# Kernel optimization log

Measured on AMD Instinct MI355X. Metric: run time of the kernel, lower is better.

The kernel has to match this reference:

```python
import jax, jax.numpy as jnp
import numpy as np

HEADS = 16  # init kwarg 'heads'

def setup_inputs() -> dict:
    key = jax.random.key(0)
    k1, k2, k3 = jax.random.split(key, 3)
    B, S, D = 2, 2048, 1024
    x = jax.random.normal(k1, (B, S, D), dtype=jnp.float32)
    # nn.Linear(dim, 3*dim, bias=False): y = x @ W^T; store as [D, 3D] already transposed.
    w_qkv = jax.random.normal(k2, (D, 3 * D), dtype=jnp.float32) * 0.02
    w_out = jax.random.normal(k3, (D, D), dtype=jnp.float32) * 0.02
    return {"x": x, "w_qkv": w_qkv, "w_out": w_out}

def reference(x, w_qkv, w_out):
    B, S, D = x.shape
    H = HEADS
    hd = D // H
    scale = 1.0 / jnp.sqrt(jnp.asarray(hd, dtype=x.dtype))
    qkv = x @ w_qkv                      # [B, S, 3D]
    q, k, v = jnp.split(qkv, 3, axis=-1)
    def to_heads(t):
        return t.reshape(B, S, H, hd).transpose(0, 2, 1, 3)  # [B, H, S, hd]
    q, k, v = to_heads(q), to_heads(k), to_heads(v)
    scores = jnp.einsum('bhqd,bhkd->bhqk', q, k) * scale      # [B, H, S, S]
    # causal mask: query i attends to keys j <= i
    causal = jnp.tril(jnp.ones((S, S), dtype=bool))
    scores = jnp.where(causal, scores, -jnp.inf)
    p = jax.nn.softmax(scores, axis=-1)  # online-softmax in the original == exact softmax
    o = jnp.einsum('bhqk,bhkd->bhqd', p, v)                   # [B, H, S, hd]
    out = o.transpose(0, 2, 1, 3).reshape(B, S, D)
    return out @ w_out
```

## Files before the change

### kernel.cpp

```cpp
#include <hip/hip_runtime.h>


typedef unsigned short u16;
typedef unsigned int   u32;
typedef __attribute__((ext_vector_type(4))) u16    u16x4;
typedef __attribute__((ext_vector_type(8))) u16    u16x8;
typedef __attribute__((ext_vector_type(4))) short  s16x4;
typedef __attribute__((ext_vector_type(8))) __bf16 bf16x8;
typedef __attribute__((ext_vector_type(4))) float  f32x4;
typedef __attribute__((ext_vector_type(16))) float f32x16;

#define DEV static __device__ __forceinline__

DEV u16 f2b(float f) {
  unsigned u = __float_as_uint(f);
  u += 0x7fffu + ((u >> 16) & 1u);
  return (u16)(u >> 16);
}

DEV void gload_lds16(const void* g, void* l) {
  __builtin_amdgcn_global_load_lds((const __attribute__((address_space(1))) void*)g,
                                   (__attribute__((address_space(3))) void*)l, 16, 0, 0);
}

DEV unsigned lds_off(const void* p) {
  return (unsigned)(unsigned long long)(const __attribute__((address_space(3))) void*)p;
}

DEV s16x4 tr_read(unsigned off) {
  s16x4 d;
  asm volatile("ds_read_b64_tr_b16 %0, %1" : "=v"(d) : "v"(off));
  return d;
}

DEV u32 cvt_pk(float lo, float hi) {
  u32 r;
  asm("v_cvt_pk_bf16_f32 %0, %1, %2" : "=v"(r) : "v"(lo), "v"(hi));
  return r;
}

DEV void pswap(u32& x, u32& y) {
  asm volatile("v_permlane32_swap_b32 %0, %1" : "+v"(x), "+v"(y));
}

DEV f32x4 mfma32(bf16x8 a, bf16x8 b, f32x4 c) {
  return __builtin_amdgcn_mfma_f32_16x16x32_bf16(a, b, c, 0, 0, 0);
}
DEV f32x16 mfma3232(bf16x8 a, bf16x8 b, f32x16 c) {
  return __builtin_amdgcn_mfma_f32_32x32x16_bf16(a, b, c, 0, 0, 0);
}

__global__ __launch_bounds__(256) void cvt_kernel(const float* __restrict__ in,
                                                  u16* __restrict__ out, int n4) {
  int i = blockIdx.x * 256 + threadIdx.x;
  if (i >= n4) return;
  const float4 v = ((const float4*)in)[i];
  u16x4 o = { f2b(v.x), f2b(v.y), f2b(v.z), f2b(v.w) };
  ((u16x4*)out)[i] = o;
}

__global__ __launch_bounds__(256) void transpose_cvt(const float* __restrict__ w,
                                                     u16* __restrict__ wt,
                                                     const int Kdim, const int Ndim,
                                                     const int scaleN) {
  __shared__ u16 ls[32][33];
  const int tn = blockIdx.x * 32, tk = blockIdx.y * 32;
  const int t = threadIdx.x;
  const int r = t >> 3, c4 = (t & 7) * 4;
  const float s = (tn < scaleN) ? 0.18033688011112042f : 1.0f;
  float4 v = *(const float4*)(w + (size_t)(tk + r) * Ndim + tn + c4);
  ls[r][c4 + 0] = f2b(v.x * s); ls[r][c4 + 1] = f2b(v.y * s);
  ls[r][c4 + 2] = f2b(v.z * s); ls[r][c4 + 3] = f2b(v.w * s);
  __syncthreads();
  u16x4 ov = { ls[c4 + 0][r], ls[c4 + 1][r], ls[c4 + 2][r], ls[c4 + 3][r] };
  *(u16x4*)(wt + (size_t)(tn + r) * Kdim + tk + c4) = ov;
}

template<bool OUT_BF16>
__global__ __launch_bounds__(256) void gemm_bt(const u16* __restrict__ A,
                                               const u16* __restrict__ Bt,
                                               void* __restrict__ C, const int ldc) {
  const int gx = gridDim.x;
  const int id = (int)(blockIdx.y * gx + blockIdx.x);
  const int nxp = gx >> 3;
  const int xcd = id & 7, loc = id >> 3;
  const int tn = (xcd * nxp + loc % nxp) * 128;
  const int tm = (loc / nxp) * 128;
  const int tid = threadIdx.x;
  const int wave = tid >> 6, lane = tid & 63;
  const int wr = wave >> 1, wc = wave & 1;
  const int lg = lane >> 4, lc = lane & 15;
  __shared__ __align__(128) u16 lsA[128 * 32];
  __shared__ __align__(128) u16 lsB[128 * 32];

  f32x4 acc[4][4];
#pragma unroll
  for (int i = 0; i < 4; ++i)
#pragma unroll
    for (int j = 0; j < 4; ++j) acc[i][j] = (f32x4){0.f, 0.f, 0.f, 0.f};

  for (int kt = 0; kt < 32; ++kt) {
#pragma unroll
    for (int c = 0; c < 2; ++c) {
      const int p = tid + c * 256;
      const int row = p >> 2, ck = p & 3;
      const int cg = ck ^ ((row >> 1) & 3);
      gload_lds16(A  + (size_t)(tm + row) * 1024 + kt * 32 + cg * 8, (char*)lsA + p * 16);
      gload_lds16(Bt + (size_t)(tn + row) * 1024 + kt * 32 + cg * 8, (char*)lsB + p * 16);
    }
    __syncthreads();
    bf16x8 af[4], bg[4];
#pragma unroll
    for (int i = 0; i < 4; ++i) {
      const int ar = wr * 64 + i * 16 + lc;
      af[i] = *(const bf16x8*)(lsA + ar * 32 + (lg ^ ((ar >> 1) & 3)) * 8);
      const int br = wc * 64 + i * 16 + lc;
      bg[i] = *(const bf16x8*)(lsB + br * 32 + (lg ^ ((br >> 1) & 3)) * 8);
    }
#pragma unroll
    for (int i = 0; i < 4; ++i)
#pragma unroll
      for (int j = 0; j < 4; ++j)
        acc[i][j] = mfma32(af[i], bg[j], acc[i][j]);
    __syncthreads();
  }

#pragma unroll
  for (int i = 0; i < 4; ++i) {
#pragma unroll
    for (int r = 0; r < 4; ++r) {
      const int m = tm + wr * 64 + i * 16 + lg * 4 + r;
#pragma unroll
      for (int j = 0; j < 4; ++j) {
        const int n = tn + wc * 64 + j * 16 + lc;
        if (OUT_BF16) ((u16*)C)[(size_t)m * ldc + n] = f2b(acc[i][j][r]);
        else          ((float*)C)[(size_t)m * ldc + n] = acc[i][j][r];
      }
    }
  }
}

__global__ __launch_bounds__(256) void gemm_bt64(const u16* __restrict__ A,
                                                 const u16* __restrict__ Bt,
                                                 float* __restrict__ C, const int ldc) {
  const int id = (int)(blockIdx.y * 8 + blockIdx.x);
  const int tn = (id & 7) * 128;
  const int tm = (id >> 3) * 64;
  const int tid = threadIdx.x;
  const int wave = tid >> 6, lane = tid & 63;
  const int wc = wave;
  const int lg = lane >> 4, lc = lane & 15;
  __shared__ __align__(128) u16 lsA[64 * 32];
  __shared__ __align__(128) u16 lsB[128 * 32];

  f32x4 acc[4][2];
#pragma unroll
  for (int i = 0; i < 4; ++i)
#pragma unroll
    for (int j = 0; j < 2; ++j) acc[i][j] = (f32x4){0.f, 0.f, 0.f, 0.f};

  for (int kt = 0; kt < 32; ++kt) {
    {
      const int p = tid;
      const int row = p >> 2, ck = p & 3;
      const int cg = ck ^ ((row >> 1) & 3);
      gload_lds16(A + (size_t)(tm + row) * 1024 + kt * 32 + cg * 8, (char*)lsA + p * 16);
    }
#pragma unroll
    for (int c = 0; c < 2; ++c) {
      const int p = tid + c * 256;
      const int row = p >> 2, ck = p & 3;
      const int cg = ck ^ ((row >> 1) & 3);
      gload_lds16(Bt + (size_t)(tn + row) * 1024 + kt * 32 + cg * 8, (char*)lsB + p * 16);
    }
    __syncthreads();
    bf16x8 af[4], bg[2];
#pragma unroll
    for (int i = 0; i < 4; ++i) {
      const int ar = i * 16 + lc;
      af[i] = *(const bf16x8*)(lsA + ar * 32 + (lg ^ ((ar >> 1) & 3)) * 8);
    }
#pragma unroll
    for (int j = 0; j < 2; ++j) {
      const int br = wc * 32 + j * 16 + lc;
      bg[j] = *(const bf16x8*)(lsB + br * 32 + (lg ^ ((br >> 1) & 3)) * 8);
    }
#pragma unroll
    for (int i = 0; i < 4; ++i)
#pragma unroll
      for (int j = 0; j < 2; ++j)
        acc[i][j] = mfma32(af[i], bg[j], acc[i][j]);
    __syncthreads();
  }

#pragma unroll
  for (int i = 0; i < 4; ++i) {
#pragma unroll
    for (int r = 0; r < 4; ++r) {
      const int m = tm + i * 16 + lg * 4 + r;
#pragma unroll
      for (int j = 0; j < 2; ++j) {
        const int n = tn + wc * 32 + j * 16 + lc;
        C[(size_t)m * ldc + n] = acc[i][j][r];
      }
    }
  }
}

__global__ __launch_bounds__(128, 2) void attn_kernel(const u16* __restrict__ qkv,
                                                      u16* __restrict__ o) {
  const int qb  = 63 - (int)(blockIdx.x >> 5);
  const int bh  = blockIdx.x & 31;
  const int b   = bh >> 4, h = bh & 15;
  const int tid  = threadIdx.x;
  const int wave = tid >> 6, lane = tid & 63;
  const int l31 = lane & 31, lg2 = lane >> 5;

  __shared__ __align__(128) char smem[2][8192];
  __shared__ float lsm[2][32];
  char* wb = smem[wave];
  const unsigned vb = lds_off(wb + 4096);

  const size_t bS = (size_t)b * 2048;
  const int T  = qb + 1;
  const int q0 = qb * 32;

  const u16* qrow = qkv + (bS + q0 + l31) * 3072 + h * 64;
  bf16x8 qf[4];
#pragma unroll
  for (int m = 0; m < 4; ++m)
    qf[m] = *(const bf16x8*)(qrow + 16 * m + 8 * lg2);

  unsigned koff[4], voff[4];
#pragma unroll
  for (int c = 0; c < 4; ++c) {
    const int p = c * 64 + lane;
    {
      const int row = p >> 3;
      const int cg = (p & 7) ^ (row & 7);
      koff[c] = (unsigned)(row * 3072 + 1024 + h * 64 + cg * 8);
    }
    {
      const int s = p >> 3, cw = p & 7;
      voff[c] = (unsigned)((4 * (s >> 2) + (cw >> 1)) * 3072 + 2048 + h * 64
                           + (s & 3) * 16 + (cw & 1) * 8);
    }
  }

  auto STAGE = [&](int t) {
    const u16* base = qkv + (bS + (size_t)t * 32) * 3072;
#pragma unroll
    for (int c = 0; c < 4; ++c)
      gload_lds16(base + koff[c], wb + (c * 64 + lane) * 16);
#pragma unroll
    for (int c = 0; c < 4; ++c)
      gload_lds16(base + voff[c], wb + 4096 + (c * 64 + lane) * 16);
  };

  float lsum = 0.f;
  f32x16 accO[2];
#pragma unroll
  for (int r = 0; r < 16; ++r) { accO[0][r] = 0.f; accO[1][r] = 0.f; }

  if (wave < T) STAGE(wave);

  for (int t = wave; t < T; t += 2) {
    asm volatile("s_waitcnt vmcnt(0)" ::: "memory");
    __builtin_amdgcn_sched_barrier(0);

    const u16* kbp = (const u16*)wb + l31 * 64;
    bf16x8 kf[4];
#pragma unroll
    for (int m = 0; m < 4; ++m)
      kf[m] = *(const bf16x8*)(kbp + (((2 * m + lg2) ^ (l31 & 7)) * 8));
    s16x4 vr[2][2][2];
#pragma unroll
    for (int db = 0; db < 2; ++db)
#pragma unroll
      for (int hh = 0; hh < 2; ++hh) {
        const unsigned a0 = vb +
          (unsigned)(((4 * hh + 2 * lg2) * 4 + db * 2 + (l31 >> 4)) * 128 + (l31 & 15) * 8);
        vr[db][hh][0] = tr_read(a0);
        vr[db][hh][1] = tr_read(a0 + 512);
      }
    asm volatile("s_waitcnt lgkmcnt(0)" ::: "memory");
    __builtin_amdgcn_sched_barrier(0);

    if (t + 2 < T) STAGE(t + 2);
    __builtin_amdgcn_sched_barrier(0);

    f32x16 sc;
#pragma unroll
    for (int r = 0; r < 16; ++r) sc[r] = 0.f;
    __builtin_amdgcn_s_setprio(1);
#pragma unroll
    for (int m = 0; m < 4; ++m)
      sc = mfma3232(kf[m], qf[m], sc);
    __builtin_amdgcn_s_setprio(0);

    float pp[16];
    if (t == T - 1) {
#pragma unroll
      for (int r = 0; r < 16; ++r) {
        const int kvp = (r & 3) + 8 * (r >> 2) + 4 * lg2;
        pp[r] = (kvp <= l31) ? exp2f(sc[r]) : 0.f;
      }
    } else {
#pragma unroll
      for (int r = 0; r < 16; ++r) pp[r] = exp2f(sc[r]);
    }
#pragma unroll
    for (int r = 0; r < 16; ++r) lsum += pp[r];

    u32 a01 = cvt_pk(pp[0], pp[1]),   a23 = cvt_pk(pp[2], pp[3]);
    u32 b01 = cvt_pk(pp[4], pp[5]),   b23 = cvt_pk(pp[6], pp[7]);
    u32 c01 = cvt_pk(pp[8], pp[9]),   c23 = cvt_pk(pp[10], pp[11]);
    u32 d01 = cvt_pk(pp[12], pp[13]), d23 = cvt_pk(pp[14], pp[15]);
    pswap(a01, b01); pswap(a23, b23);
    pswap(c01, d01); pswap(c23, d23);
    union Frag { u32 w[4]; bf16x8 v; };
    Frag f0, f1;
    f0.w[0] = a01; f0.w[1] = a23; f0.w[2] = b01; f0.w[3] = b23;
    f1.w[0] = c01; f1.w[1] = c23; f1.w[2] = d01; f1.w[3] = d23;

    __builtin_amdgcn_s_setprio(1);
#pragma unroll
    for (int db = 0; db < 2; ++db) {
      union { s16x4 hh[2]; bf16x8 v; } u0, u1;
      u0.hh[0] = vr[db][0][0]; u0.hh[1] = vr[db][0][1];
      u1.hh[0] = vr[db][1][0]; u1.hh[1] = vr[db][1][1];
      accO[db] = mfma3232(f0.v, u0.v, accO[db]);
      accO[db] = mfma3232(f1.v, u1.v, accO[db]);
    }
    __builtin_amdgcn_s_setprio(0);
  }

  lsum += __shfl_xor(lsum, 32);
  float* mO = (float*)wb;
#pragma unroll
  for (int db = 0; db < 2; ++db)
#pragma unroll
    for (int r = 0; r < 16; ++r) {
      const int qp = (r & 3) + 8 * (r >> 2) + 4 * lg2;
      mO[qp * 64 + db * 32 + l31] = accO[db][r];
    }
  if (lane < 32) lsm[wave][l31] = lsum;
  __syncthreads();

  const float* O0 = (const float*)smem[0];
  const float* O1 = (const float*)smem[1];
  const int q  = wave * 16 + (lane >> 2);
  const int d0 = (lane & 3) * 16;
  const float inv = 1.f / (lsm[0][q] + lsm[1][q]);
  u16x8 ov[2];
#pragma unroll
  for (int j = 0; j < 4; ++j) {
    const f32x4 a = *(const f32x4*)(O0 + q * 64 + d0 + j * 4);
    const f32x4 c = *(const f32x4*)(O1 + q * 64 + d0 + j * 4);
#pragma unroll
    for (int e = 0; e < 4; ++e)
      ov[j >> 1][(j & 1) * 4 + e] = f2b((a[e] + c[e]) * inv);
  }
  const size_t orow = (bS + q0 + q) * 1024 + h * 64 + d0;
  *(u16x8*)(o + orow)     = ov[0];
  *(u16x8*)(o + orow + 8) = ov[1];
}

extern "C" void kernel_launch(void* const* d_in, const int* in_sizes, int n_in,
                              void* d_out, int out_size, void* d_ws, size_t ws_size,
                              hipStream_t stream) {
  const float* x     = (const float*)d_in[0];
  const float* w_qkv = (const float*)d_in[1];
  const float* w_out = (const float*)d_in[2];
  float* out = (float*)d_out;
  char* ws = (char*)d_ws;

  u16* xb    = (u16*)(ws + 0);
  u16* wqkvT = (u16*)(ws + 8388608);
  u16* woutT = (u16*)(ws + 14680064);
  u16* qkvb  = (u16*)(ws + 16777216);
  u16* ob    = (u16*)(ws + 41943040);

  cvt_kernel<<<4096, 256, 0, stream>>>(x, xb, 1048576);
  transpose_cvt<<<dim3(96, 32), 256, 0, stream>>>(w_qkv, wqkvT, 1024, 3072, 1024);
  transpose_cvt<<<dim3(32, 32), 256, 0, stream>>>(w_out, woutT, 1024, 1024, 0);
  gemm_bt<true ><<<dim3(24, 32), 256, 0, stream>>>(xb, wqkvT, (void*)qkvb, 3072);
  attn_kernel<<<2048, 128, 0, stream>>>(qkvb, ob);
  gemm_bt64<<<dim3(8, 64), 256, 0, stream>>>(ob, woutT, out, 1024);
}
```

Baseline: 105.7 us.

## Split KV range across block pairs with paired causal q-tiles and merge pass

Each attention block now handles two query tiles (p and 63-p) to balance causal work, and the KV range of each tile is split across two blocks (four waves total) with unnormalized fp16 partials. A new attn_merge kernel sums the two partials, normalizes by the combined row sum and writes bf16 output. This targets load imbalance and tail effects of the causal triangle, at the cost of an extra kernel launch, scratch traffic and fp16 partial precision. The scratch buffers reuse the xb region of the workspace, which is assumed dead after the QKV GEMM.

```diff
diff --git a/kernel.cpp b/kernel.cpp
--- a/kernel.cpp
+++ b/kernel.cpp
@@ -16,6 +16,15 @@
   unsigned u = __float_as_uint(f);
   u += 0x7fffu + ((u >> 16) & 1u);
   return (u16)(u >> 16);
+}
+
+DEV u16 f2h(float f) {
+  _Float16 h = (_Float16)f;
+  return *(u16*)&h;
+}
+DEV float h2f(u16 u) {
+  _Float16 h = *(_Float16*)&u;
+  return (float)h;
 }
 
 DEV void gload_lds16(const void* g, void* l) {
@@ -208,12 +217,17 @@
 }
 
 __global__ __launch_bounds__(128, 2) void attn_kernel(const u16* __restrict__ qkv,
-                                                      u16* __restrict__ o) {
-  const int qb  = 63 - (int)(blockIdx.x >> 5);
-  const int bh  = blockIdx.x & 31;
+                                                      u16* __restrict__ ob,
+                                                      u16* __restrict__ scrO,
+                                                      float* __restrict__ scrL) {
+  const int id  = (int)blockIdx.x;
+  const int kh  = id & 1;
+  const int bh  = (id >> 1) & 31;
+  const int p   = id >> 6;
   const int b   = bh >> 4, h = bh & 15;
   const int tid  = threadIdx.x;
   const int wave = tid >> 6, lane = tid & 63;
+  const int slot = 2 * kh + wave;
   const int l31 = lane & 31, lg2 = lane >> 5;
 
   __shared__ __align__(128) char smem[2][8192];
@@ -222,26 +236,18 @@
   const unsigned vb = lds_off(wb + 4096);
 
   const size_t bS = (size_t)b * 2048;
-  const int T  = qb + 1;
-  const int q0 = qb * 32;
-
-  const u16* qrow = qkv + (bS + q0 + l31) * 3072 + h * 64;
-  bf16x8 qf[4];
-#pragma unroll
-  for (int m = 0; m < 4; ++m)
-    qf[m] = *(const bf16x8*)(qrow + 16 * m + 8 * lg2);
 
   unsigned koff[4], voff[4];
 #pragma unroll
   for (int c = 0; c < 4; ++c) {
-    const int p = c * 64 + lane;
+    const int pp_ = c * 64 + lane;
     {
-      const int row = p >> 3;
-      const int cg = (p & 7) ^ (row & 7);
+      const int row = pp_ >> 3;
+      const int cg = (pp_ & 7) ^ (row & 7);
       koff[c] = (unsigned)(row * 3072 + 1024 + h * 64 + cg * 8);
     }
     {
-      const int s = p >> 3, cw = p & 7;
+      const int s = pp_ >> 3, cw = pp_ & 7;
       voff[c] = (unsigned)((4 * (s >> 2) + (cw >> 1)) * 3072 + 2048 + h * 64
                            + (s & 3) * 16 + (cw & 1) * 8);
     }
@@ -257,113 +263,156 @@
       gload_lds16(base + voff[c], wb + 4096 + (c * 64 + lane) * 16);
   };
 
-  float lsum = 0.f;
-  f32x16 accO[2];
-#pragma unroll
-  for (int r = 0; r < 16; ++r) { accO[0][r] = 0.f; accO[1][r] = 0.f; }
-
-  if (wave < T) STAGE(wave);
-
-  for (int t = wave; t < T; t += 2) {
-    asm volatile("s_waitcnt vmcnt(0)" ::: "memory");
-    __builtin_amdgcn_sched_barrier(0);
-
-    const u16* kbp = (const u16*)wb + l31 * 64;
-    bf16x8 kf[4];
+  auto run_qtile = [&](int qb) {
+    const int T  = qb + 1;
+    const int q0 = qb * 32;
+
+    const u16* qrow = qkv + (bS + q0 + l31) * 3072 + h * 64;
+    bf16x8 qf[4];
 #pragma unroll
     for (int m = 0; m < 4; ++m)
-      kf[m] = *(const bf16x8*)(kbp + (((2 * m + lg2) ^ (l31 & 7)) * 8));
-    s16x4 vr[2][2][2];
+      qf[m] = *(const bf16x8*)(qrow + 16 * m + 8 * lg2);
+
+    float lsum = 0.f;
+    f32x16 accO[2];
+#pragma unroll
+    for (int r = 0; r < 16; ++r) { accO[0][r] = 0.f; accO[1][r] = 0.f; }
+
+    if (slot < T) STAGE(slot);
+
+    for (int t = slot; t < T; t += 4) {
+      asm volatile("s_waitcnt vmcnt(0)" ::: "memory");
+      __builtin_amdgcn_sched_barrier(0);
+
+      const u16* kbp = (const u16*)wb + l31 * 64;
+      bf16x8 kf[4];
+#pragma unroll
+      for (int m = 0; m < 4; ++m)
+        kf[m] = *(const bf16x8*)(kbp + (((2 * m + lg2) ^ (l31 & 7)) * 8));
+      s16x4 vr[2][2][2];
+#pragma unroll
+      for (int db = 0; db < 2; ++db)
+#pragma unroll
+        for (int hh = 0; hh < 2; ++hh) {
+          const unsigned a0 = vb +
+            (unsigned)(((4 * hh + 2 * lg2) * 4 + db * 2 + (l31 >> 4)) * 128 + (l31 & 15) * 8);
+          vr[db][hh][0] = tr_read(a0);
+          vr[db][hh][1] = tr_read(a0 + 512);
+        }
+      asm volatile("s_waitcnt lgkmcnt(0)" ::: "memory");
+      __builtin_amdgcn_sched_barrier(0);
+
+      if (t + 4 < T) STAGE(t + 4);
+      __builtin_amdgcn_sched_barrier(0);
+
+      f32x16 sc;
+#pragma unroll
+      for (int r = 0; r < 16; ++r) sc[r] = 0.f;
+      __builtin_amdgcn_s_setprio(1);
+#pragma unroll
+      for (int m = 0; m < 4; ++m)
+        sc = mfma3232(kf[m], qf[m], sc);
+      __builtin_amdgcn_s_setprio(0);
+
+      float pp[16];
+      if (t == T - 1) {
+#pragma unroll
+        for (int r = 0; r < 16; ++r) {
+          const int kvp = (r & 3) + 8 * (r >> 2) + 4 * lg2;
+          pp[r] = (kvp <= l31) ? exp2f(sc[r]) : 0.f;
+        }
+      } else {
+#pragma unroll
+        for (int r = 0; r < 16; ++r) pp[r] = exp2f(sc[r]);
+      }
+#pragma unroll
+      for (int r = 0; r < 16; ++r) lsum += pp[r];
+
+      u32 a01 = cvt_pk(pp[0], pp[1]),   a23 = cvt_pk(pp[2], pp[3]);
+      u32 b01 = cvt_pk(pp[4], pp[5]),   b23 = cvt_pk(pp[6], pp[7]);
+      u32 c01 = cvt_pk(pp[8], pp[9]),   c23 = cvt_pk(pp[10], pp[11]);
+      u32 d01 = cvt_pk(pp[12], pp[13]), d23 = cvt_pk(pp[14], pp[15]);
+      pswap(a01, b01); pswap(a23, b23);
+      pswap(c01, d01); pswap(c23, d23);
+      union Frag { u32 w[4]; bf16x8 v; };
+      Frag f0, f1;
+      f0.w[0] = a01; f0.w[1] = a23; f0.w[2] = b01; f0.w[3] = b23;
+      f1.w[0] = c01; f1.w[1] = c23; f1.w[2] = d01; f1.w[3] = d23;
+
+      __builtin_amdgcn_s_setprio(1);
+#pragma unroll
+      for (int db = 0; db < 2; ++db) {
+        union { s16x4 hh[2]; bf16x8 v; } u0, u1;
+        u0.hh[0] = vr[db][0][0]; u0.hh[1] = vr[db][0][1];
+        u1.hh[0] = vr[db][1][0]; u1.hh[1] = vr[db][1][1];
+        accO[db] = mfma3232(f0.v, u0.v, accO[db]);
+        accO[db] = mfma3232(f1.v, u1.v, accO[db]);
+      }
+      __builtin_amdgcn_s_setprio(0);
+    }
+
+    lsum += __shfl_xor(lsum, 32);
+    float* mO = (float*)wb;
 #pragma unroll
     for (int db = 0; db < 2; ++db)
 #pragma unroll
-      for (int hh = 0; hh < 2; ++hh) {
-        const unsigned a0 = vb +
-          (unsigned)(((4 * hh + 2 * lg2) * 4 + db * 2 + (l31 >> 4)) * 128 + (l31 & 15) * 8);
-        vr[db][hh][0] = tr_read(a0);
-        vr[db][hh][1] = tr_read(a0 + 512);
+      for (int r = 0; r < 16; ++r) {
+        const int qp = (r & 3) + 8 * (r >> 2) + 4 * lg2;
+        mO[qp * 64 + db * 32 + l31] = accO[db][r];
       }
-    asm volatile("s_waitcnt lgkmcnt(0)" ::: "memory");
-    __builtin_amdgcn_sched_barrier(0);
-
-    if (t + 2 < T) STAGE(t + 2);
-    __builtin_amdgcn_sched_barrier(0);
-
-    f32x16 sc;
-#pragma unroll
-    for (int r = 0; r < 16; ++r) sc[r] = 0.f;
-    __builtin_amdgcn_s_setprio(1);
-#pragma unroll
-    for (int m = 0; m < 4; ++m)
-      sc = mfma3232(kf[m], qf[m], sc);
-    __builtin_amdgcn_s_setprio(0);
-
-    float pp[16];
-    if (t == T - 1) {
-#pragma unroll
-      for (int r = 0; r < 16; ++r) {
-        const int kvp = (r & 3) + 8 * (r >> 2) + 4 * lg2;
-        pp[r] = (kvp <= l31) ? exp2f(sc[r]) : 0.f;
-      }
-    } else {
-#pragma unroll
-      for (int r = 0; r < 16; ++r) pp[r] = exp2f(sc[r]);
-    }
-#pragma unroll
-    for (int r = 0; r < 16; ++r) lsum += pp[r];
-
-    u32 a01 = cvt_pk(pp[0], pp[1]),   a23 = cvt_pk(pp[2], pp[3]);
-    u32 b01 = cvt_pk(pp[4], pp[5]),   b23 = cvt_pk(pp[6], pp[7]);
-    u32 c01 = cvt_pk(pp[8], pp[9]),   c23 = cvt_pk(pp[10], pp[11]);
-    u32 d01 = cvt_pk(pp[12], pp[13]), d23 = cvt_pk(pp[14], pp[15]);
-    pswap(a01, b01); pswap(a23, b23);
-    pswap(c01, d01); pswap(c23, d23);
-    union Frag { u32 w[4]; bf16x8 v; };
-    Frag f0, f1;
-    f0.w[0] = a01; f0.w[1] = a23; f0.w[2] = b01; f0.w[3] = b23;
-    f1.w[0] = c01; f1.w[1] = c23; f1.w[2] = d01; f1.w[3] = d23;
-
-    __builtin_amdgcn_s_setprio(1);
-#pragma unroll
-    for (int db = 0; db < 2; ++db) {
-      union { s16x4 hh[2]; bf16x8 v; } u0, u1;
-      u0.hh[0] = vr[db][0][0]; u0.hh[1] = vr[db][0][1];
-      u1.hh[0] = vr[db][1][0]; u1.hh[1] = vr[db][1][1];
-      accO[db] = mfma3232(f0.v, u0.v, accO[db]);
-      accO[db] = mfma3232(f1.v, u1.v, accO[db]);
-    }
-    __builtin_amdgcn_s_setprio(0);
-  }
-
-  lsum += __shfl_xor(lsum, 32);
-  float* mO = (float*)wb;
-#pragma unroll
-  for (int db = 0; db < 2; ++db)
-#pragma unroll
-    for (int r = 0; r < 16; ++r) {
-      const int qp = (r & 3) + 8 * (r >> 2) + 4 * lg2;
-      mO[qp * 64 + db * 32 + l31] = accO[db][r];
-    }
-  if (lane < 32) lsm[wave][l31] = lsum;
-  __syncthreads();
-
-  const float* O0 = (const float*)smem[0];
-  const float* O1 = (const float*)smem[1];
-  const int q  = wave * 16 + (lane >> 2);
-  const int d0 = (lane & 3) * 16;
-  const float inv = 1.f / (lsm[0][q] + lsm[1][q]);
-  u16x8 ov[2];
-#pragma unroll
-  for (int j = 0; j < 4; ++j) {
-    const f32x4 a = *(const f32x4*)(O0 + q * 64 + d0 + j * 4);
-    const f32x4 c = *(const f32x4*)(O1 + q * 64 + d0 + j * 4);
-#pragma unroll
-    for (int e = 0; e < 4; ++e)
-      ov[j >> 1][(j & 1) * 4 + e] = f2b((a[e] + c[e]) * inv);
-  }
-  const size_t orow = (bS + q0 + q) * 1024 + h * 64 + d0;
-  *(u16x8*)(o + orow)     = ov[0];
-  *(u16x8*)(o + orow + 8) = ov[1];
+    if (lane < 32) lsm[wave][l31] = lsum;
+    __syncthreads();
+
+    const float* O0 = (const float*)smem[0];
+    const float* O1 = (const float*)smem[1];
+    const int q  = wave * 16 + (lane >> 2);
+    const int d0 = (lane & 3) * 16;
+    const float lpart = lsm[0][q] + lsm[1][q];
+    u16x8 ov[2];
+#pragma unroll
+    for (int j = 0; j < 4; ++j) {
+      const f32x4 a = *(const f32x4*)(O0 + q * 64 + d0 + j * 4);
+      const f32x4 c = *(const f32x4*)(O1 + q * 64 + d0 + j * 4);
+#pragma unroll
+      for (int e = 0; e < 4; ++e)
+        ov[j >> 1][(j & 1) * 4 + e] = f2h(a[e] + c[e]);
+    }
+    const int combo = qb * 32 + bh;
+    u16* dst = (kh == 0)
+      ? ob + (bS + q0 + q) * 1024 + h * 64 + d0
+      : scrO + ((size_t)combo * 32 + q) * 64 + d0;
+    *(u16x8*)dst = ov[0];
+    *(u16x8*)(dst + 8) = ov[1];
+    if ((lane & 3) == 0) scrL[kh * 65536 + combo * 32 + q] = lpart;
+    __syncthreads();
+  };
+
+  run_qtile(p);
+  run_qtile(63 - p);
+}
+
+__global__ __launch_bounds__(128) void attn_merge(u16* __restrict__ ob,
+                                                  const u16* __restrict__ scrO,
+                                                  const float* __restrict__ scrL) {
+  const int id = (int)blockIdx.x;
+  const int qb = id >> 5, bh = id & 31;
+  const int b = bh >> 4, h = bh & 15;
+  const int q  = (int)(threadIdx.x >> 2);
+  const int d0 = ((int)threadIdx.x & 3) * 16;
+  const float l = scrL[id * 32 + q] + scrL[65536 + id * 32 + q];
+  const float inv = 1.f / l;
+  u16* dst = ob + ((size_t)b * 2048 + qb * 32 + q) * 1024 + h * 64 + d0;
+  const u16* src1 = scrO + ((size_t)id * 32 + q) * 64 + d0;
+  u16x8 p0a = *(const u16x8*)dst,       p0b = *(const u16x8*)(dst + 8);
+  u16x8 p1a = *(const u16x8*)src1,      p1b = *(const u16x8*)(src1 + 8);
+  u16x8 oa, obv;
+#pragma unroll
+  for (int e = 0; e < 8; ++e) {
+    oa[e]  = f2b((h2f(p0a[e]) + h2f(p1a[e])) * inv);
+    obv[e] = f2b((h2f(p0b[e]) + h2f(p1b[e])) * inv);
+  }
+  *(u16x8*)dst       = oa;
+  *(u16x8*)(dst + 8) = obv;
 }
 
 extern "C" void kernel_launch(void* const* d_in, const int* in_sizes, int n_in,
@@ -380,11 +429,14 @@
   u16* woutT = (u16*)(ws + 14680064);
   u16* qkvb  = (u16*)(ws + 16777216);
   u16* ob    = (u16*)(ws + 41943040);
+  u16*   scrO = (u16*)(ws + 0);
+  float* scrL = (float*)(ws + 8912896);
 
   cvt_kernel<<<4096, 256, 0, stream>>>(x, xb, 1048576);
   transpose_cvt<<<dim3(96, 32), 256, 0, stream>>>(w_qkv, wqkvT, 1024, 3072, 1024);
   transpose_cvt<<<dim3(32, 32), 256, 0, stream>>>(w_out, woutT, 1024, 1024, 0);
   gemm_bt<true ><<<dim3(24, 32), 256, 0, stream>>>(xb, wqkvT, (void*)qkvb, 3072);
-  attn_kernel<<<2048, 128, 0, stream>>>(qkvb, ob);
+  attn_kernel<<<2048, 128, 0, stream>>>(qkvb, ob, scrO, scrL);
+  attn_merge<<<2048, 128, 0, stream>>>(ob, scrO, scrL);
   gemm_bt64<<<dim3(8, 64), 256, 0, stream>>>(ob, woutT, out, 1024);
 }
```

Measured after the change: 120.4 us. 1.14x slower.
